# Kernel optimization log

Hardware: AMD Instinct MI355X
Metric: run time of the kernel (lower is better)

## Reference

```python
import jax, jax.numpy as jnp
import numpy as np
from jax import lax

ROPE_THETA = 10000.0


def rotate_half(x):
    d = x.shape[-1] // 2
    return jnp.concatenate([-x[..., d:], x[..., :d]], axis=-1)


def segsum(x):
    # x: (..., l) -> (..., l, l) lower-triangular segment sums (off-tri = -inf)
    T = x.shape[-1]
    cs = jnp.cumsum(x, axis=-1)
    d = cs[..., :, None] - cs[..., None, :]
    mask = jnp.tril(jnp.ones((T, T), dtype=bool))
    return jnp.where(mask, d, -jnp.inf)


def setup_inputs() -> dict:
    key = jax.random.key(0)
    ks = jax.random.split(key, 8)
    B, L, D, H = 2, 8192, 1024, 16
    P = D // H  # head_dim == state_dim
    hidden_states = jax.random.normal(ks[0], (B, L, D), dtype=jnp.float32)
    # rotary embeddings over head_dim
    inv_freq = 1.0 / (ROPE_THETA ** (np.arange(0, P, 2, dtype=np.float32) / P))
    pos = np.arange(L, dtype=np.float32)
    freqs = pos[:, None] * inv_freq[None, :]            # (L, P/2)
    emb = np.concatenate([freqs, freqs], axis=-1)       # (L, P)
    cos = jnp.asarray(np.broadcast_to(np.cos(emb), (B, L, P)).copy())
    sin = jnp.asarray(np.broadcast_to(np.sin(emb), (B, L, P)).copy())
    s = 1.0 / np.sqrt(D)
    Wc = jax.random.normal(ks[1], (D, D), dtype=jnp.float32) * s
    Wb = jax.random.normal(ks[2], (D, D), dtype=jnp.float32) * s
    Wx = jax.random.normal(ks[3], (D, D), dtype=jnp.float32) * s
    Wdt = jax.random.normal(ks[4], (D, H), dtype=jnp.float32) * s
    Wout = jax.random.normal(ks[5], (D, D), dtype=jnp.float32) * s
    # A must be negative for a stable decaying SSM (Mamba2 convention A = -exp(A_log))
    A = -(0.5 + jax.random.uniform(ks[6], (H,), dtype=jnp.float32))
    return {"hidden_states": hidden_states, "cos": cos, "sin": sin,
            "Wc": Wc, "Wb": Wb, "Wdt": Wdt, "Wx": Wx, "Wout": Wout,
            "A": A, "chunk_size": 256}


def reference(hidden_states, cos, sin, Wc, Wb, Wdt, Wx, Wout, A, chunk_size):
    B, L, D = hidden_states.shape
    H = A.shape[0]
    P = D // H
    nc = L // chunk_size
    cl = chunk_size

    c = (hidden_states @ Wc).reshape(B, L, H, P)
    b = (hidden_states @ Wb).reshape(B, L, H, P)
    x = (hidden_states @ Wx).reshape(B, L, H, P)
    dt = jax.nn.softplus(hidden_states @ Wdt)  # (B, L, H), dt_softplus=True

    # rotary on C and B (unsqueeze_dim=2)
    cosu, sinu = cos[:, :, None, :], sin[:, :, None, :]
    c = c * cosu + rotate_half(c) * sinu
    b = b * cosu + rotate_half(b) * sinu

    # chunked SSD (mamba_chunk_scan_combined)
    cr = c.reshape(B, nc, cl, H, P)
    br = b.reshape(B, nc, cl, H, P)
    xdt = (x * dt[..., None]).reshape(B, nc, cl, H, P)
    dA = (dt * A[None, None, :]).reshape(B, nc, cl, H)
    dAc = jnp.transpose(dA, (0, 3, 1, 2))            # (B, H, nc, cl)
    Acum = jnp.cumsum(dAc, axis=-1)                  # (B, H, nc, cl)

    # intra-chunk (diagonal) term
    Lmask = jnp.exp(segsum(dAc))                     # (B, H, nc, cl, cl)
    Y_diag = jnp.einsum('bclhn,bcshn,bhcls,bcshp->bclhp', cr, br, Lmask, xdt)

    # per-chunk states
    decay_states = jnp.exp(Acum[..., -1:] - Acum)    # (B, H, nc, cl)
    states = jnp.einsum('bclhn,bhcl,bclhp->bchpn', br, decay_states, xdt)
    chunk_decay = jnp.exp(Acum[..., -1])             # (B, H, nc)

    def step(h, inp):
        s, dec = inp                                 # (B,H,P,N), (B,H)
        h_new = h * dec[..., None, None] + s
        return h_new, h                              # emit state BEFORE this chunk

    states_c = jnp.moveaxis(states, 1, 0)            # (nc, B, H, P, N)
    dec_c = jnp.moveaxis(chunk_decay, 2, 0)          # (nc, B, H)
    h0 = jnp.zeros((B, H, P, P), dtype=hidden_states.dtype)
    final_state, prev_states = lax.scan(step, h0, (states_c, dec_c))
    prev_states = jnp.moveaxis(prev_states, 0, 1)    # (B, nc, H, P, N)

    # inter-chunk (off-diagonal) term
    state_decay_out = jnp.exp(Acum)                  # (B, H, nc, cl)
    Y_off = jnp.einsum('bclhn,bchpn,bhcl->bclhp', cr, prev_states, state_decay_out)

    y = (Y_diag + Y_off).reshape(B, L, D)
    out = y @ Wout
    return out, final_state
```

## Files before the change

kernel.cpp:

```cpp
#include <hip/hip_runtime.h>
#include <hip/hip_bf16.h>

typedef unsigned short u16;

#define Bb 2
#define Ll 8192
#define Dd 1024
#define Hh 16
#define Pp 64
#define CLc 256
#define NCc 32
#define Mm 16384
#define DD2 ((size_t)Dd*Dd)
#define WDTSZ ((size_t)256*1024)

typedef __attribute__((ext_vector_type(8))) short short8b;
typedef __attribute__((ext_vector_type(4))) float f32x4v;

__device__ __forceinline__ float bf2f(u16 u){
    return __uint_as_float(((unsigned int)u) << 16);
}
__device__ __forceinline__ u16 f2bf(float f){
    unsigned int i = __float_as_uint(f);
    unsigned int r = (i + 0x7FFFu + ((i >> 16) & 1u)) >> 16;
    return (u16)r;
}

template<int DT>
__device__ __forceinline__ void ld8(const void* p, size_t i, float* o){
    if (DT){
        const u16* q = (const u16*)p + i;
        ushort4 a0 = *(const ushort4*)q;
        ushort4 a1 = *(const ushort4*)(q + 4);
        o[0]=bf2f(a0.x); o[1]=bf2f(a0.y); o[2]=bf2f(a0.z); o[3]=bf2f(a0.w);
        o[4]=bf2f(a1.x); o[5]=bf2f(a1.y); o[6]=bf2f(a1.z); o[7]=bf2f(a1.w);
    } else {
        const float* q = (const float*)p + i;
        float4 a0 = *(const float4*)q;
        float4 a1 = *(const float4*)(q + 4);
        o[0]=a0.x; o[1]=a0.y; o[2]=a0.z; o[3]=a0.w;
        o[4]=a1.x; o[5]=a1.y; o[6]=a1.z; o[7]=a1.w;
    }
}
__device__ __forceinline__ float ldf(const void* p, size_t i, int dtf){
    return dtf ? bf2f(((const u16*)p)[i]) : ((const float*)p)[i];
}

typedef __attribute__((address_space(3))) void lds_t;
typedef __attribute__((address_space(1))) const void gm_t;
__device__ __forceinline__ void gload16(const void* g, void* l){
    __builtin_amdgcn_global_load_lds((gm_t*)g, (lds_t*)l, 16, 0, 0);
}

__device__ __forceinline__ void fence_barrier(){
    asm volatile("" ::: "memory");
    __builtin_amdgcn_s_barrier();
    asm volatile("" ::: "memory");
}

__global__ void sniff_kernel(const unsigned int* __restrict__ cosw, int* __restrict__ flag){
    if (threadIdx.x == 0 && blockIdx.x == 0)
        *flag = (cosw[0] == 0x3F800000u) ? 0 : 1;
}

__global__ __launch_bounds__(256) void cospack_kernel(
    const void* __restrict__ cosb, const void* __restrict__ sinb,
    float* __restrict__ cp, const int* __restrict__ flag)
{
    const int dtf = *flag;
    int i = blockIdx.x*256 + threadIdx.x;
    int tok = i >> 6, c = i & 63;
    float v = (c < 32) ? ldf(cosb, (size_t)tok*64 + c,        dtf)
                       : ldf(sinb, (size_t)tok*64 + (c - 32), dtf);
    cp[i] = v;
}

__global__ __launch_bounds__(256) void cvt_kernel(
    const void* __restrict__ in, u16* __restrict__ out, const int* __restrict__ flag)
{
    const int dtf = *flag;
    size_t i = ((size_t)blockIdx.x*256 + threadIdx.x) * 8;
    float v[8];
    if (dtf) ld8<1>(in, i, v); else ld8<0>(in, i, v);
    ushort4 o0, o1;
    o0.x=f2bf(v[0]); o0.y=f2bf(v[1]); o0.z=f2bf(v[2]); o0.w=f2bf(v[3]);
    o1.x=f2bf(v[4]); o1.y=f2bf(v[5]); o1.z=f2bf(v[6]); o1.w=f2bf(v[7]);
    *(ushort4*)(out + i)     = o0;
    *(ushort4*)(out + i + 4) = o1;
}

__global__ __launch_bounds__(256) void wtrans_kernel(
    const void* __restrict__ W0, const void* __restrict__ W1,
    const void* __restrict__ W2, const void* __restrict__ W3,
    u16* __restrict__ out, const int* __restrict__ flag)
{
    const int dtf = *flag;
    const int z = blockIdx.z;
    const void* W = (z==0) ? W0 : (z==1) ? W1 : (z==2) ? W2 : W3;
    u16* Whi = out + (size_t)z*DD2 + (z==3 ? WDTSZ : 0);
    u16* Wlo = out + (size_t)4*DD2 + WDTSZ;
    __shared__ u16 th[64][65];
    __shared__ u16 tlo[64][65];
    const int t = threadIdx.x;
    const int r = t >> 2, cq = (t & 3)*16;
    size_t base = ((size_t)blockIdx.y*64 + r)*1024 + (size_t)blockIdx.x*64 + cq;
    float v[8];
#pragma unroll
    for (int half = 0; half < 2; half++){
        if (dtf) ld8<1>(W, base + half*8, v); else ld8<0>(W, base + half*8, v);
#pragma unroll
        for (int j = 0; j < 8; j++){
            u16 hi = f2bf(v[j]);
            th[r][cq + half*8 + j]  = hi;
            tlo[r][cq + half*8 + j] = f2bf(v[j] - bf2f(hi));
        }
    }
    __syncthreads();
    size_t ob = ((size_t)blockIdx.x*64 + r)*1024 + (size_t)blockIdx.y*64 + cq;
#pragma unroll
    for (int j = 0; j < 16; j++)
        Whi[ob + j] = th[cq + j][r];
    if (z == 3){
#pragma unroll
        for (int j = 0; j < 16; j++)
            Wlo[ob + j] = tlo[cq + j][r];
    }
}

__global__ __launch_bounds__(256) void wdtrep_kernel(
    const void* __restrict__ Wdt, u16* __restrict__ wdt, const int* __restrict__ flag)
{
    const int dtf = *flag;
    int i = blockIdx.x*256 + threadIdx.x;
    int r = i >> 10, k = i & 1023;
    wdt[i] = f2bf(ldf(Wdt, (size_t)k*16 + (r & 15), dtf));
}

template<int DTC, int ACC, int FUSE>
__global__ __launch_bounds__(512) void gemm_mfma(
    const u16* __restrict__ A, const u16* __restrict__ Bt, void* __restrict__ C,
    int M, int N, int K, const int* __restrict__ flag, int want,
    const float* __restrict__ cp, float* __restrict__ dtb)
{
    if (want >= 0 && *flag != want) return;
    __shared__ __align__(128) u16 As[4][256*32];
    __shared__ __align__(128) u16 Bs[4][256*32];
    const int t    = threadIdx.x;
    const int wave = t >> 6;
    const int lane = t & 63;

    const int nbn = N >> 8;
    const int nbm = M >> 8;
    int wg = blockIdx.x, nwg = gridDim.x;
    int bm, bn;
    if ((nwg & 7) == 0 && (nbm & 7) == 0){
        const int x   = wg & 7;
        const int loc = wg >> 3;
        const int rpx = nbm >> 3;
        const int bmL = loc % rpx;
        bn = loc / rpx;
        bm = x*rpx + bmL;
    } else {
        bm = wg / nbn; bn = wg % nbn;
    }

    const int ldrow = wave*16 + (lane >> 2);
    const int ldk   = (lane & 3)*8;
    const u16* Ag0 = A  + (size_t)(bm*256 + ldrow)*K + ldk;
    const u16* Ag1 = Ag0 + (size_t)128*K;
    const u16* Bg0 = Bt + (size_t)(bn*256 + ldrow)*K + ldk;
    const u16* Bg1 = Bg0 + (size_t)128*K;
    const int o0 = (wave*16)*32;
    const int o1 = (128 + wave*16)*32;

    const int wr = wave >> 2, wc = wave & 3;
    const int fr = lane & 15;
    const int fk = (lane >> 4)*8;

    f32x4v acc[8][4] = {};

    const int steps = K >> 5;
#pragma unroll
    for (int s = 0; s < 2; s++){
        gload16(Ag0 + s*32, &As[s][o0]);
        gload16(Ag1 + s*32, &As[s][o1]);
        gload16(Bg0 + s*32, &Bs[s][o0]);
        gload16(Bg1 + s*32, &Bs[s][o1]);
    }

    for (int ts = 0; ts < steps; ++ts){
        if (ts + 2 < steps){
            const int sb = (ts + 2) & 3;
            const int ko = (ts + 2)*32;
            gload16(Ag0 + ko, &As[sb][o0]);
            gload16(Ag1 + ko, &As[sb][o1]);
            gload16(Bg0 + ko, &Bs[sb][o0]);
            gload16(Bg1 + ko, &Bs[sb][o1]);
            asm volatile("s_waitcnt vmcnt(8)" ::: "memory");
        } else if (ts + 1 < steps){
            asm volatile("s_waitcnt vmcnt(4)" ::: "memory");
        } else {
            asm volatile("s_waitcnt vmcnt(0)" ::: "memory");
        }
        fence_barrier();
        const int cb = ts & 3;
        const u16* a_rd = &As[cb][(wr*128 + fr)*32 + fk];
        const u16* b_rd = &Bs[cb][(wc*64 + fr)*32 + fk];
        short8b af[8], bfv[4];
#pragma unroll
        for (int i = 0; i < 8; i++)
            af[i]  = *(const short8b*)(a_rd + i*16*32);
#pragma unroll
        for (int i = 0; i < 4; i++)
            bfv[i] = *(const short8b*)(b_rd + i*16*32);
#pragma unroll
        for (int mi = 0; mi < 8; mi++)
#pragma unroll
            for (int ni = 0; ni < 4; ni++)
                acc[mi][ni] = __builtin_amdgcn_mfma_f32_16x16x32_bf16(
                    af[mi], bfv[ni], acc[mi][ni], 0, 0, 0);
    }

    const int crow = (lane >> 4)*4;
    const int ccol = lane & 15;

    if (FUSE && bn == nbn - 1){
        if (wc == 0){
#pragma unroll
            for (int mi = 0; mi < 8; mi++){
#pragma unroll
                for (int r = 0; r < 4; r++){
                    size_t row = (size_t)bm*256 + wr*128 + mi*16 + crow + r;
                    float v = acc[mi][0][r];
                    float sp = (v > 20.f) ? v : log1pf(__expf(v));
                    dtb[row*16 + ccol] = sp;
                }
            }
        }
        return;
    }

    const int bufid = FUSE ? (bn >> 2) : 0;
    const int bnl   = FUSE ? (bn & 3) : bn;
    u16* Cf = FUSE ? ((u16*)C + (size_t)bufid*((size_t)Mm*Dd)) : (u16*)C;
    const size_t Nout = FUSE ? (size_t)Dd : (size_t)N;

    if (FUSE && bufid < 2){
#pragma unroll
        for (int mi = 0; mi < 8; mi++){
#pragma unroll
            for (int r = 0; r < 4; r++){
                size_t row = (size_t)bm*256 + wr*128 + mi*16 + crow + r;
                const float* cpr = cp + (size_t)(row & (Ll-1))*64;
                float cs0 = cpr[ccol],      cs1 = cpr[ccol + 16];
                float sn0 = cpr[32 + ccol], sn1 = cpr[48 + ccol];
                float a0 = acc[mi][0][r], a1 = acc[mi][1][r];
                float a2 = acc[mi][2][r], a3 = acc[mi][3][r];
                acc[mi][0][r] = a0*cs0 - a2*sn0;
                acc[mi][2][r] = a2*cs0 + a0*sn0;
                acc[mi][1][r] = a1*cs1 - a3*sn1;
                acc[mi][3][r] = a3*cs1 + a1*sn1;
            }
        }
    }

#pragma unroll
    for (int mi = 0; mi < 8; mi++){
#pragma unroll
        for (int ni = 0; ni < 4; ni++){
            size_t col = (size_t)bnl*256 + wc*64 + ni*16 + ccol;
#pragma unroll
            for (int r = 0; r < 4; r++){
                size_t row = (size_t)bm*256 + wr*128 + mi*16 + crow + r;
                float v = acc[mi][ni][r];
                if (DTC){
                    Cf[row*Nout + col] = f2bf(v);
                } else {
                    float* p = (float*)C + row*Nout + col;
                    *p = ACC ? (*p + v) : v;
                }
            }
        }
    }
}

__global__ __launch_bounds__(256) void chunk_kernel(
    const u16* __restrict__ cr, u16* brY, const u16* __restrict__ xd,
    float* __restrict__ Acum, float* __restrict__ states,
    const float* __restrict__ dtb, const void* __restrict__ Aarr,
    const int* __restrict__ flag)
{
    __shared__ u16 brs[256*72];
    __shared__ u16 brTs[64*264];
    __shared__ u16 xdsT[64*264];
    __shared__ u16 plds[4][64*72];
    __shared__ float acs[256];
    __shared__ float wexp[256];
    const int dtf = *flag;
    const int g = blockIdx.x;
    const int h = g & 15, c = (g >> 4) & 31, b = g >> 9;
    const int t = threadIdx.x;
    const int wv = t >> 6, lane = t & 63;
    const size_t tokbase = (size_t)b*Ll + (size_t)c*CLc;
    float* Acw = Acum + ((size_t)(b*Hh + h)*NCc + c)*CLc;

    acs[t] = dtb[(tokbase + t)*Hh + h] * ldf(Aarr, h, dtf);
    __syncthreads();
    for (int off = 1; off < 256; off <<= 1){
        float add = (t >= off) ? acs[t - off] : 0.f;
        __syncthreads();
        acs[t] += add;
        __syncthreads();
    }
    const float a_last = acs[255];
    wexp[t] = __expf(fminf(a_last - acs[t], 0.f));
    Acw[t] = acs[t];
    __syncthreads();

#pragma unroll
    for (int i = 0; i < 8; i++){
        int f8 = i*256 + t;
        int l  = f8 >> 3;
        int n8 = (f8 & 7)*8;
        size_t goff = (tokbase + l)*Dd + h*Pp + n8;
        ushort4 a0 = *(const ushort4*)&brY[goff];
        ushort4 a1 = *(const ushort4*)&brY[goff + 4];
        *(ushort4*)&brs[l*72 + n8]     = a0;
        *(ushort4*)&brs[l*72 + n8 + 4] = a1;
        float wl = wexp[l];
        u16 bv[8] = {(u16)a0.x,(u16)a0.y,(u16)a0.z,(u16)a0.w,
                     (u16)a1.x,(u16)a1.y,(u16)a1.z,(u16)a1.w};
#pragma unroll
        for (int j = 0; j < 8; j++)
            brTs[(n8 + j)*264 + l] = f2bf(wl * bf2f(bv[j]));
        float dl = dtb[(tokbase + l)*Hh + h];
        ushort4 x0 = *(const ushort4*)&xd[goff];
        ushort4 x1 = *(const ushort4*)&xd[goff + 4];
        u16 xv[8] = {(u16)x0.x,(u16)x0.y,(u16)x0.z,(u16)x0.w,
                     (u16)x1.x,(u16)x1.y,(u16)x1.z,(u16)x1.w};
#pragma unroll
        for (int j = 0; j < 8; j++)
            xdsT[(n8 + j)*264 + l] = f2bf(bf2f(xv[j]) * dl);
    }
    __syncthreads();

    const int fr = lane & 15;
    const int kb = (lane >> 4)*8;

    {
        int ks0 = 0;
        for (int ks = 0; ks < 8; ks++){
            if (a_last - acs[ks*32 + 31] >= -30.f){ ks0 = ks; break; }
        }
        f32x4v sacc[4] = {};
        const int pr = wv*16 + fr;
        for (int ks = ks0; ks < 8; ks++){
            short8b afr = *(const short8b*)&xdsT[pr*264 + ks*32 + kb];
#pragma unroll
            for (int ni = 0; ni < 4; ni++){
                short8b bfr = *(const short8b*)&brTs[(ni*16 + fr)*264 + ks*32 + kb];
                sacc[ni] = __builtin_amdgcn_mfma_f32_16x16x32_bf16(afr, bfr, sacc[ni], 0, 0, 0);
            }
        }
        float* st = states + ((size_t)((b*NCc + c)*Hh) + h)*4096;
        const int prow = wv*16 + (lane >> 4)*4;
#pragma unroll
        for (int ni = 0; ni < 4; ni++)
#pragma unroll
            for (int r = 0; r < 4; r++)
                st[(prow + r)*64 + ni*16 + fr] = sacc[ni][r];
    }

    {
        short8b crf[4][2];
#pragma unroll
        for (int mi = 0; mi < 4; mi++)
#pragma unroll
            for (int ks = 0; ks < 2; ks++)
                crf[mi][ks] = *(const short8b*)&cr[(tokbase + wv*64 + mi*16 + fr)*Dd + h*Pp + ks*32 + kb];

        float al[4][4];
#pragma unroll
        for (int mi = 0; mi < 4; mi++)
#pragma unroll
            for (int r = 0; r < 4; r++)
                al[mi][r] = acs[wv*64 + mi*16 + (lane >> 4)*4 + r];

        f32x4v yacc[4][4] = {};
        u16* pw = &plds[wv][0];
        const float a_hi = acs[wv*64];

        for (int cb = wv; cb >= 0; --cb){
            if (a_hi - acs[cb*64 + 63] < -30.f) break;
#pragma unroll
            for (int mi = 0; mi < 4; mi++){
#pragma unroll
                for (int ni = 0; ni < 4; ni++){
                    f32x4v s4 = {};
#pragma unroll
                    for (int ks = 0; ks < 2; ks++){
                        short8b bfr = *(const short8b*)&brs[(cb*64 + ni*16 + fr)*72 + ks*32 + kb];
                        s4 = __builtin_amdgcn_mfma_f32_16x16x32_bf16(crf[mi][ks], bfr, s4, 0, 0, 0);
                    }
                    const int s_idx = cb*64 + ni*16 + fr;
                    const float a_s = acs[s_idx];
                    const int lrow0 = wv*64 + mi*16 + (lane >> 4)*4;
#pragma unroll
                    for (int r = 0; r < 4; r++){
                        float w  = __expf(fminf(al[mi][r] - a_s, 0.f));
                        float pv = (s_idx <= lrow0 + r) ? w * s4[r] : 0.f;
                        pw[(mi*16 + (lane >> 4)*4 + r)*72 + ni*16 + fr] = f2bf(pv);
                    }
                }
            }
            asm volatile("s_waitcnt lgkmcnt(0)" ::: "memory");
#pragma unroll
            for (int ks = 0; ks < 2; ks++){
                short8b paf[4];
#pragma unroll
                for (int mi = 0; mi < 4; mi++)
                    paf[mi] = *(const short8b*)&pw[(mi*16 + fr)*72 + ks*32 + kb];
#pragma unroll
                for (int pi = 0; pi < 4; pi++){
                    short8b xbf = *(const short8b*)&xdsT[(pi*16 + fr)*264 + cb*64 + ks*32 + kb];
#pragma unroll
                    for (int mi = 0; mi < 4; mi++)
                        yacc[mi][pi] = __builtin_amdgcn_mfma_f32_16x16x32_bf16(paf[mi], xbf, yacc[mi][pi], 0, 0, 0);
                }
            }
        }
#pragma unroll
        for (int mi = 0; mi < 4; mi++){
            const int lrow = wv*64 + mi*16 + (lane >> 4)*4;
#pragma unroll
            for (int r = 0; r < 4; r++){
                u16* yp = brY + (tokbase + lrow + r)*Dd + h*Pp + fr;
#pragma unroll
                for (int pi = 0; pi < 4; pi++)
                    yp[pi*16] = f2bf(yacc[mi][pi][r]);
            }
        }
    }
}

__global__ __launch_bounds__(256) void scan_kernel(
    float* st, const float* __restrict__ Acum, void* d_out, const int* __restrict__ flag)
{
    const int dtf = *flag;
    const int g = blockIdx.x;
    const int seg = g & 15;
    const int bh = g >> 4;
    const int h = bh & 15, b = bh >> 4;
    const int e = seg*256 + threadIdx.x;
    const float* Ac = Acum + (size_t)(b*Hh + h)*NCc*CLc;
    float hst = 0.f;
    for (int c = 0; c < NCc; c++){
        float dec = __expf(fminf(Ac[c*CLc + 255], 0.f));
        size_t off = ((size_t)((b*NCc + c)*Hh) + h)*4096 + e;
        float s_val = st[off];
        st[off] = hst;
        hst = hst*dec + s_val;
    }
    size_t fi = (size_t)Mm*Dd + (size_t)(b*Hh + h)*4096 + e;
    if (dtf) ((u16*)d_out)[fi] = f2bf(hst);
    else     ((float*)d_out)[fi] = hst;
}

__global__ __launch_bounds__(256) void yoff_kernel(
    const u16* __restrict__ cr, const float* __restrict__ prev,
    const float* __restrict__ Acum, u16* y)
{
    __shared__ u16 pvb[64*72];
    __shared__ float acs[256];
    const int g = blockIdx.x;
    const int h = g & 15, c = (g >> 4) & 31, b = g >> 9;
    const int t = threadIdx.x;
    const int wv = t >> 6, lane = t & 63;
    const size_t tokbase = (size_t)b*Ll + (size_t)c*CLc;
    const float* pv = prev + ((size_t)((b*NCc + c)*Hh) + h)*4096;
    const float* Ac = Acum + ((size_t)(b*Hh + h)*NCc + c)*CLc;
    acs[t] = Ac[t];
#pragma unroll
    for (int i = 0; i < 16; i++){
        int f = i*256 + t;
        int p = f >> 6, n = f & 63;
        pvb[p*72 + n] = f2bf(pv[f]);
    }
    __syncthreads();

    const int fr = lane & 15;
    const int kb = (lane >> 4)*8;

    short8b crf[4][2];
#pragma unroll
    for (int mi = 0; mi < 4; mi++)
#pragma unroll
        for (int ks = 0; ks < 2; ks++)
            crf[mi][ks] = *(const short8b*)&cr[(tokbase + wv*64 + mi*16 + fr)*Dd + h*Pp + ks*32 + kb];

    f32x4v yacc[4][4] = {};
#pragma unroll
    for (int ks = 0; ks < 2; ks++){
        short8b pbf[4];
#pragma unroll
        for (int pi = 0; pi < 4; pi++)
            pbf[pi] = *(const short8b*)&pvb[(pi*16 + fr)*72 + ks*32 + kb];
#pragma unroll
        for (int mi = 0; mi < 4; mi++)
#pragma unroll
            for (int pi = 0; pi < 4; pi++)
                yacc[mi][pi] = __builtin_amdgcn_mfma_f32_16x16x32_bf16(
                    crf[mi][ks], pbf[pi], yacc[mi][pi], 0, 0, 0);
    }

    const int crw = (lane >> 4)*4;
#pragma unroll
    for (int mi = 0; mi < 4; mi++){
        const int lrow = wv*64 + mi*16 + crw;
#pragma unroll
        for (int r = 0; r < 4; r++){
            float el = __expf(fminf(acs[lrow + r], 0.f));
            u16* yp = y + (tokbase + lrow + r)*Dd + h*Pp + fr;
#pragma unroll
            for (int pi = 0; pi < 4; pi++){
                float cur = bf2f(yp[pi*16]);
                yp[pi*16] = f2bf(cur + el*yacc[mi][pi][r]);
            }
        }
    }
}

__global__ __launch_bounds__(256) void zero_out_kernel(void* o, long long n, const int* flag)
{
    long long i = (long long)blockIdx.x*256 + threadIdx.x;
    if (i < n){
        if (*flag) ((u16*)o)[i] = 0;
        else       ((float*)o)[i] = 0.f;
    }
}

extern "C" void kernel_launch(void* const* d_in, const int* in_sizes, int n_in,
                              void* d_out, int out_size, void* d_ws, size_t ws_size,
                              hipStream_t stream)
{
    const void* hs   = d_in[0];
    const void* cosb = d_in[1];
    const void* sinb = d_in[2];
    const void* Wc   = d_in[3];
    const void* Wb   = d_in[4];
    const void* Wdt  = d_in[5];
    const void* Wx   = d_in[6];
    const void* Wout = d_in[7];
    const void* Aarr = d_in[8];

    int*  flag  = (int*)d_ws;
    char* wbase = (char*)d_ws + 1024;

    const size_t NEED = 1024
                      + (size_t)3*Mm*Dd*2
                      + (size_t)Mm*Hh*4
                      + (size_t)Bb*Hh*Ll*4
                      + (size_t)Bb*NCc*Hh*4096*4
                      + (size_t)Mm*Dd*2
                      + ((size_t)5*DD2 + WDTSZ)*2
                      + (size_t)Ll*64*4;

    sniff_kernel<<<1, 64, 0, stream>>>((const unsigned int*)cosb, flag);

    if (ws_size < NEED){
        long long n = (long long)out_size;
        zero_out_kernel<<<(unsigned)((n + 255)/256), 256, 0, stream>>>(d_out, n, flag);
        return;
    }

    u16*   c_buf  = (u16*)wbase;
    u16*   b_buf  = c_buf + (size_t)Mm*Dd;
    u16*   x_buf  = b_buf + (size_t)Mm*Dd;
    float* dt_buf = (float*)(x_buf + (size_t)Mm*Dd);
    float* acum   = dt_buf + (size_t)Mm*Hh;
    float* states = acum + (size_t)Bb*Hh*Ll;
    u16*   hs_bf  = (u16*)(states + (size_t)Bb*NCc*Hh*4096);
    u16*   wt     = hs_bf + (size_t)Mm*Dd;
    float* cp     = (float*)(wt + (size_t)5*DD2 + WDTSZ);

    cvt_kernel<<<(Mm*Dd)/(256*8), 256, 0, stream>>>(hs, hs_bf, flag);
    wtrans_kernel<<<dim3(16,16,4), 256, 0, stream>>>(Wc, Wb, Wx, Wout, wt, flag);
    wdtrep_kernel<<<(256*1024)/256, 256, 0, stream>>>(Wdt, wt + 3*DD2, flag);
    cospack_kernel<<<(Ll*64)/256, 256, 0, stream>>>(cosb, sinb, cp, flag);

    gemm_mfma<1,0,1><<<(Mm/256)*(3328/256), 512, 0, stream>>>(
        hs_bf, wt, c_buf, Mm, 3328, Dd, flag, -1, cp, dt_buf);

    chunk_kernel<<<Bb*NCc*Hh, 256, 0, stream>>>(c_buf, b_buf, x_buf, acum, states, dt_buf, Aarr, flag);
    scan_kernel<<<Bb*Hh*16, 256, 0, stream>>>(states, acum, d_out, flag);
    yoff_kernel<<<Bb*NCc*Hh, 256, 0, stream>>>(c_buf, states, acum, b_buf);

    const int NWG = (Mm/256)*(Dd/256);
    u16* woutT = wt + 3*DD2 + WDTSZ;
    u16* woutL = wt + 4*DD2 + WDTSZ;
    gemm_mfma<1,0,0><<<NWG, 512, 0, stream>>>(b_buf, woutT, d_out, Mm, Dd, Dd, flag, 1, nullptr, nullptr);
    gemm_mfma<0,0,0><<<NWG, 512, 0, stream>>>(b_buf, woutT, d_out, Mm, Dd, Dd, flag, 0, nullptr, nullptr);
    gemm_mfma<0,1,0><<<NWG, 512, 0, stream>>>(b_buf, woutL, d_out, Mm, Dd, Dd, flag, 0, nullptr, nullptr);
}
```

Baseline: 488.2 us.

## Widen chunk kernel to 512 threads and skip bf16 conversion for bf16 inputs

The chunk kernel now runs 8 waves per block instead of 4. Each wave handles 32 rows of the intra-chunk product and half the state tile, which raises occupancy and splits the triangular work more finely. Separately, when the input is already bf16 (flag==1), the conversion kernel exits early and the fused projection GEMM reads the raw hidden states directly, saving a full copy pass. In the default fp32 path only the chunk-kernel split applies; the extra waves could add LDS pressure and leave some waves with more triangular blocks than others.

```diff
diff --git a/kernel.cpp b/kernel.cpp
--- a/kernel.cpp
+++ b/kernel.cpp
@@ -78,10 +78,10 @@
 __global__ __launch_bounds__(256) void cvt_kernel(
     const void* __restrict__ in, u16* __restrict__ out, const int* __restrict__ flag)
 {
-    const int dtf = *flag;
+    if (*flag == 1) return;
     size_t i = ((size_t)blockIdx.x*256 + threadIdx.x) * 8;
     float v[8];
-    if (dtf) ld8<1>(in, i, v); else ld8<0>(in, i, v);
+    ld8<0>(in, i, v);
     ushort4 o0, o1;
     o0.x=f2bf(v[0]); o0.y=f2bf(v[1]); o0.z=f2bf(v[2]); o0.w=f2bf(v[3]);
     o1.x=f2bf(v[4]); o1.y=f2bf(v[5]); o1.z=f2bf(v[6]); o1.w=f2bf(v[7]);
@@ -138,11 +138,14 @@
 
 template<int DTC, int ACC, int FUSE>
 __global__ __launch_bounds__(512) void gemm_mfma(
-    const u16* __restrict__ A, const u16* __restrict__ Bt, void* __restrict__ C,
+    const u16* __restrict__ Abf, const void* __restrict__ Araw,
+    const u16* __restrict__ Bt, void* __restrict__ C,
     int M, int N, int K, const int* __restrict__ flag, int want,
     const float* __restrict__ cp, float* __restrict__ dtb)
 {
-    if (want >= 0 && *flag != want) return;
+    const int dtf = *flag;
+    if (want >= 0 && dtf != want) return;
+    const u16* A = (FUSE && dtf) ? (const u16*)Araw : Abf;
     __shared__ __align__(128) u16 As[4][256*32];
     __shared__ __align__(128) u16 Bs[4][256*32];
     const int t    = threadIdx.x;
@@ -284,7 +287,7 @@
     }
 }
 
-__global__ __launch_bounds__(256) void chunk_kernel(
+__global__ __launch_bounds__(512) void chunk_kernel(
     const u16* __restrict__ cr, u16* brY, const u16* __restrict__ xd,
     float* __restrict__ Acum, float* __restrict__ states,
     const float* __restrict__ dtb, const void* __restrict__ Aarr,
@@ -293,33 +296,36 @@
     __shared__ u16 brs[256*72];
     __shared__ u16 brTs[64*264];
     __shared__ u16 xdsT[64*264];
-    __shared__ u16 plds[4][64*72];
+    __shared__ u16 plds[8][32*72];
     __shared__ float acs[256];
     __shared__ float wexp[256];
     const int dtf = *flag;
     const int g = blockIdx.x;
     const int h = g & 15, c = (g >> 4) & 31, b = g >> 9;
     const int t = threadIdx.x;
-    const int wv = t >> 6, lane = t & 63;
+    const int w = t >> 6, lane = t & 63;
     const size_t tokbase = (size_t)b*Ll + (size_t)c*CLc;
     float* Acw = Acum + ((size_t)(b*Hh + h)*NCc + c)*CLc;
 
-    acs[t] = dtb[(tokbase + t)*Hh + h] * ldf(Aarr, h, dtf);
+    if (t < 256)
+        acs[t] = dtb[(tokbase + t)*Hh + h] * ldf(Aarr, h, dtf);
     __syncthreads();
     for (int off = 1; off < 256; off <<= 1){
-        float add = (t >= off) ? acs[t - off] : 0.f;
+        float add = (t < 256 && t >= off) ? acs[t - off] : 0.f;
         __syncthreads();
-        acs[t] += add;
+        if (t < 256) acs[t] += add;
         __syncthreads();
     }
     const float a_last = acs[255];
-    wexp[t] = __expf(fminf(a_last - acs[t], 0.f));
-    Acw[t] = acs[t];
+    if (t < 256){
+        wexp[t] = __expf(fminf(a_last - acs[t], 0.f));
+        Acw[t] = acs[t];
+    }
     __syncthreads();
 
 #pragma unroll
-    for (int i = 0; i < 8; i++){
-        int f8 = i*256 + t;
+    for (int i = 0; i < 4; i++){
+        int f8 = i*512 + t;
         int l  = f8 >> 3;
         int n8 = (f8 & 7)*8;
         size_t goff = (tokbase + l)*Dd + h*Pp + n8;
@@ -352,48 +358,50 @@
         for (int ks = 0; ks < 8; ks++){
             if (a_last - acs[ks*32 + 31] >= -30.f){ ks0 = ks; break; }
         }
-        f32x4v sacc[4] = {};
-        const int pr = wv*16 + fr;
+        const int pi  = w >> 1;
+        const int ni0 = (w & 1)*2;
+        f32x4v sacc[2] = {};
+        const int pr = pi*16 + fr;
         for (int ks = ks0; ks < 8; ks++){
             short8b afr = *(const short8b*)&xdsT[pr*264 + ks*32 + kb];
 #pragma unroll
-            for (int ni = 0; ni < 4; ni++){
-                short8b bfr = *(const short8b*)&brTs[(ni*16 + fr)*264 + ks*32 + kb];
-                sacc[ni] = __builtin_amdgcn_mfma_f32_16x16x32_bf16(afr, bfr, sacc[ni], 0, 0, 0);
+            for (int q = 0; q < 2; q++){
+                short8b bfr = *(const short8b*)&brTs[((ni0+q)*16 + fr)*264 + ks*32 + kb];
+                sacc[q] = __builtin_amdgcn_mfma_f32_16x16x32_bf16(afr, bfr, sacc[q], 0, 0, 0);
             }
         }
         float* st = states + ((size_t)((b*NCc + c)*Hh) + h)*4096;
-        const int prow = wv*16 + (lane >> 4)*4;
-#pragma unroll
-        for (int ni = 0; ni < 4; ni++)
+        const int prow = pi*16 + (lane >> 4)*4;
+#pragma unroll
+        for (int q = 0; q < 2; q++)
 #pragma unroll
             for (int r = 0; r < 4; r++)
-                st[(prow + r)*64 + ni*16 + fr] = sacc[ni][r];
+                st[(prow + r)*64 + (ni0+q)*16 + fr] = sacc[q][r];
     }
 
     {
-        short8b crf[4][2];
-#pragma unroll
-        for (int mi = 0; mi < 4; mi++)
+        short8b crf[2][2];
+#pragma unroll
+        for (int mi = 0; mi < 2; mi++)
 #pragma unroll
             for (int ks = 0; ks < 2; ks++)
-                crf[mi][ks] = *(const short8b*)&cr[(tokbase + wv*64 + mi*16 + fr)*Dd + h*Pp + ks*32 + kb];
-
-        float al[4][4];
-#pragma unroll
-        for (int mi = 0; mi < 4; mi++)
+                crf[mi][ks] = *(const short8b*)&cr[(tokbase + w*32 + mi*16 + fr)*Dd + h*Pp + ks*32 + kb];
+
+        float al[2][4];
+#pragma unroll
+        for (int mi = 0; mi < 2; mi++)
 #pragma unroll
             for (int r = 0; r < 4; r++)
-                al[mi][r] = acs[wv*64 + mi*16 + (lane >> 4)*4 + r];
-
-        f32x4v yacc[4][4] = {};
-        u16* pw = &plds[wv][0];
-        const float a_hi = acs[wv*64];
-
-        for (int cb = wv; cb >= 0; --cb){
+                al[mi][r] = acs[w*32 + mi*16 + (lane >> 4)*4 + r];
+
+        f32x4v yacc[2][4] = {};
+        u16* pw = &plds[w][0];
+        const float a_hi = acs[w*32];
+
+        for (int cb = w >> 1; cb >= 0; --cb){
             if (a_hi - acs[cb*64 + 63] < -30.f) break;
 #pragma unroll
-            for (int mi = 0; mi < 4; mi++){
+            for (int mi = 0; mi < 2; mi++){
 #pragma unroll
                 for (int ni = 0; ni < 4; ni++){
                     f32x4v s4 = {};
@@ -404,11 +412,11 @@
                     }
                     const int s_idx = cb*64 + ni*16 + fr;
                     const float a_s = acs[s_idx];
-                    const int lrow0 = wv*64 + mi*16 + (lane >> 4)*4;
+                    const int lrow0 = w*32 + mi*16 + (lane >> 4)*4;
 #pragma unroll
                     for (int r = 0; r < 4; r++){
-                        float w  = __expf(fminf(al[mi][r] - a_s, 0.f));
-                        float pv = (s_idx <= lrow0 + r) ? w * s4[r] : 0.f;
+                        float wgt = __expf(fminf(al[mi][r] - a_s, 0.f));
+                        float pv  = (s_idx <= lrow0 + r) ? wgt * s4[r] : 0.f;
                         pw[(mi*16 + (lane >> 4)*4 + r)*72 + ni*16 + fr] = f2bf(pv);
                     }
                 }
@@ -416,22 +424,22 @@
             asm volatile("s_waitcnt lgkmcnt(0)" ::: "memory");
 #pragma unroll
             for (int ks = 0; ks < 2; ks++){
-                short8b paf[4];
-#pragma unroll
-                for (int mi = 0; mi < 4; mi++)
+                short8b paf[2];
+#pragma unroll
+                for (int mi = 0; mi < 2; mi++)
                     paf[mi] = *(const short8b*)&pw[(mi*16 + fr)*72 + ks*32 + kb];
 #pragma unroll
                 for (int pi = 0; pi < 4; pi++){
                     short8b xbf = *(const short8b*)&xdsT[(pi*16 + fr)*264 + cb*64 + ks*32 + kb];
 #pragma unroll
-                    for (int mi = 0; mi < 4; mi++)
+                    for (int mi = 0; mi < 2; mi++)
                         yacc[mi][pi] = __builtin_amdgcn_mfma_f32_16x16x32_bf16(paf[mi], xbf, yacc[mi][pi], 0, 0, 0);
                 }
             }
         }
 #pragma unroll
-        for (int mi = 0; mi < 4; mi++){
-            const int lrow = wv*64 + mi*16 + (lane >> 4)*4;
+        for (int mi = 0; mi < 2; mi++){
+            const int lrow = w*32 + mi*16 + (lane >> 4)*4;
 #pragma unroll
             for (int r = 0; r < 4; r++){
                 u16* yp = brY + (tokbase + lrow + r)*Dd + h*Pp + fr;
@@ -589,16 +597,16 @@
     cospack_kernel<<<(Ll*64)/256, 256, 0, stream>>>(cosb, sinb, cp, flag);
 
     gemm_mfma<1,0,1><<<(Mm/256)*(3328/256), 512, 0, stream>>>(
-        hs_bf, wt, c_buf, Mm, 3328, Dd, flag, -1, cp, dt_buf);
-
-    chunk_kernel<<<Bb*NCc*Hh, 256, 0, stream>>>(c_buf, b_buf, x_buf, acum, states, dt_buf, Aarr, flag);
+        hs_bf, hs, wt, c_buf, Mm, 3328, Dd, flag, -1, cp, dt_buf);
+
+    chunk_kernel<<<Bb*NCc*Hh, 512, 0, stream>>>(c_buf, b_buf, x_buf, acum, states, dt_buf, Aarr, flag);
     scan_kernel<<<Bb*Hh*16, 256, 0, stream>>>(states, acum, d_out, flag);
     yoff_kernel<<<Bb*NCc*Hh, 256, 0, stream>>>(c_buf, states, acum, b_buf);
 
     const int NWG = (Mm/256)*(Dd/256);
     u16* woutT = wt + 3*DD2 + WDTSZ;
     u16* woutL = wt + 4*DD2 + WDTSZ;
-    gemm_mfma<1,0,0><<<NWG, 512, 0, stream>>>(b_buf, woutT, d_out, Mm, Dd, Dd, flag, 1, nullptr, nullptr);
-    gemm_mfma<0,0,0><<<NWG, 512, 0, stream>>>(b_buf, woutT, d_out, Mm, Dd, Dd, flag, 0, nullptr, nullptr);
-    gemm_mfma<0,1,0><<<NWG, 512, 0, stream>>>(b_buf, woutL, d_out, Mm, Dd, Dd, flag, 0, nullptr, nullptr);
-}
+    gemm_mfma<1,0,0><<<NWG, 512, 0, stream>>>(b_buf, nullptr, woutT, d_out, Mm, Dd, Dd, flag, 1, nullptr, nullptr);
+    gemm_mfma<0,0,0><<<NWG, 512, 0, stream>>>(b_buf, nullptr, woutT, d_out, Mm, Dd, Dd, flag, 0, nullptr, nullptr);
+    gemm_mfma<0,1,0><<<NWG, 512, 0, stream>>>(b_buf, nullptr, woutL, d_out, Mm, Dd, Dd, flag, 0, nullptr, nullptr);
+}
```

New measurement: 478.7 us, median of 2. Within noise of the previous version (-1.9%).
